# Performance work log

Hardware: AMD Instinct MI355X
Metric: run time of the kernel (lower is better)

## Reference

```python
import jax, jax.numpy as jnp
import numpy as np

# Model constants (from init_kwargs / opt)
DELTT = 4.0          # time step between dynamic frames (s)
N_TIME = 60          # number of dynamic frames
TR = 5.0             # repetition time (ms)
FA = 10.0            # flip angle (degrees)
R1 = 4.5             # contrast agent relaxivity
SCALE_KTRANS = 1.0
SCALE_VP = 1.0
EPS = 1e-8


def setup_inputs() -> dict:
    key = jax.random.key(0)
    k1, k2, k3, k4 = jax.random.split(key, 4)
    B, T, H, W = 4, N_TIME, 256, 256
    params = jax.random.uniform(k1, (B, 2, H, W), dtype=jnp.float32)   # [Ktrans; vp] maps
    Cp = jax.random.uniform(k2, (B, T), dtype=jnp.float32)             # arterial input function
    S0 = jax.random.uniform(k3, (B, 1, H, W), dtype=jnp.float32)       # equilibrium signal map
    T1 = jax.random.uniform(k4, (B, 1, H, W), dtype=jnp.float32)       # T1 relaxation map
    return {"params": params, "Cp": Cp, "S0": S0, "T1": T1}


def reference(params, Cp, S0, T1):
    # Pharmacokinetic parameter maps: [B,1,H,W]
    Ktrans = params[:, 0:1, :, :] / SCALE_KTRANS / 60.0
    vp = params[:, 1:2, :, :] / SCALE_VP

    # The original O(T^2) loop Ce[:,n] = sum(Cp[:,:n+1]) * deltt is a prefix sum.
    Ce = jnp.cumsum(Cp, axis=1) * DELTT                # [B,T]

    # Broadcast AIF over spatial dims instead of materializing .expand copies.
    Cp_b = Cp[:, :, None, None]                        # [B,T,1,1]
    Ce_b = Ce[:, :, None, None]                        # [B,T,1,1]

    Ct = vp * Cp_b + Ktrans * Ce_b                     # [B,T,H,W] tissue concentration

    # SPGR signal equation
    P = TR / (T1 + EPS)                                # [B,1,H,W]
    Q = R1 * (TR / 1000.0) * Ct                        # [B,T,H,W]
    cos_fa = np.cos(FA * np.pi / 180.0).astype(np.float32)
    exp_P = jnp.exp(-P)
    exp_PQ = jnp.exp(-P - Q)
    St = (1.0 - exp_PQ) * (1.0 - cos_fa * exp_P) / ((1.0 - cos_fa * exp_PQ) * (1.0 - exp_P) + EPS) * S0
    return St
```

## Files before the change

kernel.cpp:

```cpp
#include <hip/hip_runtime.h>


#define HW_   (256 * 256)
#define NT_   60

__global__ __launch_bounds__(256) void patlak_kernel(
    const float* __restrict__ params,
    const float* __restrict__ Cp,
    const float* __restrict__ S0,
    const float* __restrict__ T1,
    float* __restrict__ out)
{
    __shared__ float s_cp[NT_];

    const int gid = blockIdx.x * 256 + threadIdx.x;
    const int b   = gid >> 16;
    const int p   = gid & (HW_ - 1);

    if (threadIdx.x < NT_) s_cp[threadIdx.x] = Cp[b * NT_ + threadIdx.x];
    __syncthreads();

    const float pk = params[(b * 2 + 0) * HW_ + p];
    const float vp = params[(b * 2 + 1) * HW_ + p];
    const float s0 = S0[b * HW_ + p];
    const float t1 = T1[b * HW_ + p];

    const float ktD   = pk * (4.0f / 60.0f);
    const float P     = 5.0f / (t1 + 1e-8f);
    const float expP  = __expf(-P);
    const float cosfa = 0.9848077530122080594f;
    const float A     = (1.0f - cosfa * expP) * s0;
    const float omp   = 1.0f - expP;
    const float B     = omp + 1e-8f;
    const float C     = cosfa * omp;

    float ce = 0.0f;
    float* outp = out + (size_t)b * NT_ * HW_ + p;

    #pragma unroll 4
    for (int t = 0; t < NT_; ++t) {
        const float cp = s_cp[t];
        ce += cp;
        const float Ct  = vp * cp + ktD * ce;
        const float e   = __expf(-P - 0.0225f * Ct);
        const float num = A - A * e;
        const float den = B - C * e;
        outp[(size_t)t * HW_] = num * __builtin_amdgcn_rcpf(den);
    }
}

extern "C" void kernel_launch(void* const* d_in, const int* in_sizes, int n_in,
                              void* d_out, int out_size, void* d_ws, size_t ws_size,
                              hipStream_t stream) {
    const float* params = (const float*)d_in[0];
    const float* Cp     = (const float*)d_in[1];
    const float* S0     = (const float*)d_in[2];
    const float* T1     = (const float*)d_in[3];
    float* out          = (float*)d_out;

    const int total  = 4 * HW_;
    const int blocks = total / 256;
    patlak_kernel<<<blocks, 256, 0, stream>>>(params, Cp, S0, T1, out);
}
```

Before: 83.38 us.

## Split time into chunks with shared prefix-sum and vectorize 4 pixels per thread

Each thread now handles four adjacent pixels with float4 loads and stores, and the 60 frames are split into four chunks of 15 handled by different blocks. Each block computes the Cp prefix sum once with a wavefront shuffle scan into shared memory, so chunks can start mid-sequence. Grid stays at 1024 blocks, but each thread does a quarter of the time steps for four pixels. This aims at wider stores and more memory-level parallelism, at the cost of re-reading the input maps once per chunk.

```diff
diff --git a/kernel.cpp b/kernel.cpp
--- a/kernel.cpp
+++ b/kernel.cpp
@@ -3,6 +3,8 @@
 
 #define HW_   (256 * 256)
 #define NT_   60
+#define TCH_  15
+#define PXT_  4
 
 __global__ __launch_bounds__(256) void patlak_kernel(
     const float* __restrict__ params,
@@ -12,40 +14,75 @@
     float* __restrict__ out)
 {
     __shared__ float s_cp[NT_];
+    __shared__ float s_ce[NT_];
 
-    const int gid = blockIdx.x * 256 + threadIdx.x;
-    const int b   = gid >> 16;
-    const int p   = gid & (HW_ - 1);
+    const int bid = blockIdx.x;
+    const int b   = bid >> 8;
+    const int rem = bid & 255;
+    const int c   = rem >> 6;
+    const int blk = rem & 63;
+    const int tid = threadIdx.x;
 
-    if (threadIdx.x < NT_) s_cp[threadIdx.x] = Cp[b * NT_ + threadIdx.x];
+    if (tid < 64) {
+        float v = (tid < NT_) ? Cp[b * NT_ + tid] : 0.0f;
+        float s = v;
+        #pragma unroll
+        for (int d = 1; d < 64; d <<= 1) {
+            float u = __shfl_up(s, d, 64);
+            if (tid >= d) s += u;
+        }
+        if (tid < NT_) { s_cp[tid] = v; s_ce[tid] = s; }
+    }
     __syncthreads();
 
-    const float pk = params[(b * 2 + 0) * HW_ + p];
-    const float vp = params[(b * 2 + 1) * HW_ + p];
-    const float s0 = S0[b * HW_ + p];
-    const float t1 = T1[b * HW_ + p];
+    const int p4 = (blk * 256 + tid) * PXT_;
 
-    const float ktD   = pk * (4.0f / 60.0f);
-    const float P     = 5.0f / (t1 + 1e-8f);
-    const float expP  = __expf(-P);
+    const float4 kt4 = *(const float4*)(params + (size_t)(b * 2 + 0) * HW_ + p4);
+    const float4 vp4 = *(const float4*)(params + (size_t)(b * 2 + 1) * HW_ + p4);
+    const float4 s04 = *(const float4*)(S0 + (size_t)b * HW_ + p4);
+    const float4 t14 = *(const float4*)(T1 + (size_t)b * HW_ + p4);
+
     const float cosfa = 0.9848077530122080594f;
-    const float A     = (1.0f - cosfa * expP) * s0;
-    const float omp   = 1.0f - expP;
-    const float B     = omp + 1e-8f;
-    const float C     = cosfa * omp;
 
-    float ce = 0.0f;
-    float* outp = out + (size_t)b * NT_ * HW_ + p;
+    float kD[PXT_], vp[PXT_], P[PXT_], A[PXT_], Bv[PXT_], Cv[PXT_];
+    {
+        const float kt_[4] = {kt4.x, kt4.y, kt4.z, kt4.w};
+        const float vp_[4] = {vp4.x, vp4.y, vp4.z, vp4.w};
+        const float s0_[4] = {s04.x, s04.y, s04.z, s04.w};
+        const float t1_[4] = {t14.x, t14.y, t14.z, t14.w};
+        #pragma unroll
+        for (int i = 0; i < PXT_; ++i) {
+            kD[i] = kt_[i] * (4.0f / 60.0f);
+            vp[i] = vp_[i];
+            P[i]  = 5.0f / (t1_[i] + 1e-8f);
+            const float ep  = __expf(-P[i]);
+            const float omp = 1.0f - ep;
+            A[i]  = (1.0f - cosfa * ep) * s0_[i];
+            Bv[i] = omp + 1e-8f;
+            Cv[i] = cosfa * omp;
+        }
+    }
 
-    #pragma unroll 4
-    for (int t = 0; t < NT_; ++t) {
-        const float cp = s_cp[t];
-        ce += cp;
-        const float Ct  = vp * cp + ktD * ce;
-        const float e   = __expf(-P - 0.0225f * Ct);
-        const float num = A - A * e;
-        const float den = B - C * e;
-        outp[(size_t)t * HW_] = num * __builtin_amdgcn_rcpf(den);
+    const int t0 = c * TCH_;
+    float* outp = out + ((size_t)b * NT_ + t0) * HW_ + p4;
+
+    #pragma unroll 5
+    for (int i = 0; i < TCH_; ++i) {
+        const float cp = s_cp[t0 + i];
+        const float ce = s_ce[t0 + i];
+        float4 r;
+        float res[PXT_];
+        #pragma unroll
+        for (int j = 0; j < PXT_; ++j) {
+            const float Ct = vp[j] * cp + kD[j] * ce;
+            const float e  = __expf(-P[j] - 0.0225f * Ct);
+            const float num = A[j] - A[j] * e;
+            const float den = Bv[j] - Cv[j] * e;
+            res[j] = num * __builtin_amdgcn_rcpf(den);
+        }
+        r.x = res[0]; r.y = res[1]; r.z = res[2]; r.w = res[3];
+        *(float4*)outp = r;
+        outp += HW_;
     }
 }
 
@@ -58,7 +95,5 @@
     const float* T1     = (const float*)d_in[3];
     float* out          = (float*)d_out;
 
-    const int total  = 4 * HW_;
-    const int blocks = total / 256;
-    patlak_kernel<<<blocks, 256, 0, stream>>>(params, Cp, S0, T1, out);
+    patlak_kernel<<<1024, 256, 0, stream>>>(params, Cp, S0, T1, out);
 }
```

New measurement: 82.01 us. Within noise of the previous version (-1.6%).
